# Optimization experiments

Hardware: AMD Instinct MI355X
Metric: run time of the kernel (lower is better)

The kernel has to match this reference:

```python
import jax, jax.numpy as jnp
import numpy as np

B, NQ, NKV = 2, 2048, 2048
DIM, CTX_DIM = 1024, 1024
HEADS, DIM_HEAD = 16, 64
INNER = HEADS * DIM_HEAD  # 1024
SCALE = DIM_HEAD ** -0.5


def setup_inputs() -> dict:
    key = jax.random.key(0)
    ks = jax.random.split(key, 6)
    x = jax.random.normal(ks[0], (B, NQ, DIM), dtype=jnp.float32)
    context = jax.random.normal(ks[1], (B, NKV, CTX_DIM), dtype=jnp.float32)
    # nn.Linear weights stored as [out, in] in torch; we keep [in, out] for x @ W.
    Wq = jax.random.normal(ks[2], (DIM, INNER), dtype=jnp.float32) / np.sqrt(DIM)
    Wkv = jax.random.normal(ks[3], (CTX_DIM, 2 * INNER), dtype=jnp.float32) / np.sqrt(CTX_DIM)
    Wout = jax.random.normal(ks[4], (INNER, DIM), dtype=jnp.float32) / np.sqrt(INNER)
    bout = jax.random.normal(ks[5], (DIM,), dtype=jnp.float32) * 0.01
    return {"x": x, "context": context, "Wq": Wq, "Wkv": Wkv, "Wout": Wout, "bout": bout}


def reference(x, context, Wq, Wkv, Wout, bout):
    q = x @ Wq                      # [B, Nq, inner]
    kv = context @ Wkv              # [B, Nkv, 2*inner]
    k, v = jnp.split(kv, 2, axis=-1)

    def split_heads(t):             # [B, N, inner] -> [B, H, N, dh]
        return t.reshape(t.shape[0], t.shape[1], HEADS, DIM_HEAD).transpose(0, 2, 1, 3)

    q, k, v = split_heads(q), split_heads(k), split_heads(v)
    dots = jnp.einsum('bhqd,bhkd->bhqk', q, k) * SCALE  # [B, H, Nq, Nkv]
    attn = jax.nn.softmax(dots, axis=-1)
    out = jnp.einsum('bhqk,bhkd->bhqd', attn, v)        # [B, H, Nq, dh]
    out = out.transpose(0, 2, 1, 3).reshape(out.shape[0], out.shape[2], INNER)
    return out @ Wout + bout        # [B, Nq, dim]
```

## Files before the change

### kernel.cpp

```cpp
#include <hip/hip_runtime.h>
#include <hip/hip_bf16.h>
#include <stdint.h>

#define NQ 2048
#define NKV 2048
#define DIM 1024
#define INNER 1024
#define HEADS 16
#define DH 64
#define BATCH 2

typedef float f32x4 __attribute__((ext_vector_type(4)));
typedef float f32x16 __attribute__((ext_vector_type(16)));
typedef __bf16 bf16x8 __attribute__((ext_vector_type(8)));
typedef unsigned int u32x4 __attribute__((ext_vector_type(4)));

__device__ inline ushort f2b(float f) {
    uint32_t u = __builtin_bit_cast(uint32_t, f);
    u += 0x7fff + ((u >> 16) & 1);
    return (ushort)(u >> 16);
}

__device__ inline uint pkbf16(float lo, float hi) {
    __hip_bfloat162 h = __float22bfloat162_rn(make_float2(lo, hi));
    uint r;
    __builtin_memcpy(&r, &h, 4);
    return r;
}

__device__ __forceinline__ void gload16(const void* g, void* lds) {
    __builtin_amdgcn_global_load_lds(
        (const __attribute__((address_space(1))) unsigned int*)g,
        (__attribute__((address_space(3))) unsigned int*)lds, 16, 0, 0);
}

__global__ void prep(const float* __restrict__ x, const float* __restrict__ ctx,
                     const float* __restrict__ Wq, const float* __restrict__ Wkv,
                     const float* __restrict__ Wout,
                     ushort* __restrict__ xb, ushort* __restrict__ cb,
                     ushort* __restrict__ Wqt, ushort* __restrict__ Wkvt,
                     ushort* __restrict__ Woutt) {
    int z = blockIdx.z;
    if (z < 4) {
        __shared__ ushort tile[32][33];
        const float* src; ushort* dst; int C;
        if (z == 0)      { src = Wq;          dst = Wqt;                C = 1024; }
        else if (z == 1) { src = Wkv;         dst = Wkvt;               C = 2048; }
        else if (z == 2) { src = Wkv + 1024;  dst = Wkvt + 1024 * 1024; C = 2048; }
        else             { src = Wout;        dst = Woutt;              C = 1024; }
        int c0 = blockIdx.x * 32, r0 = blockIdx.y * 32;
        int tx = threadIdx.x, ty = threadIdx.y;
#pragma unroll
        for (int i = 0; i < 4; i++)
            tile[ty + i * 8][tx] = f2b(src[(size_t)(r0 + ty + i * 8) * C + c0 + tx]);
        __syncthreads();
#pragma unroll
        for (int i = 0; i < 4; i++)
            dst[(size_t)(c0 + ty + i * 8) * 1024 + r0 + tx] = tile[tx][ty + i * 8];
    } else {
        const int n4 = (BATCH * NQ * DIM) / 4;
        int fb = blockIdx.y * 32 + blockIdx.x;
        int t = threadIdx.y * 32 + threadIdx.x;
        for (int i = fb * 256 + t; i < 2 * n4; i += 1024 * 256) {
            float4 v;
            if (i < n4) v = ((const float4*)x)[i];
            else        v = ((const float4*)ctx)[i - n4];
            ushort4 o;
            o.x = f2b(v.x); o.y = f2b(v.y); o.z = f2b(v.z); o.w = f2b(v.w);
            if (i < n4) ((ushort4*)xb)[i] = o;
            else        ((ushort4*)cb)[i - n4] = o;
        }
    }
}

__global__ __launch_bounds__(256) void gemm_qkv(const ushort* __restrict__ xb, const ushort* __restrict__ cb,
                                                const ushort* __restrict__ Wqt, const ushort* __restrict__ Wkvt,
                                                ushort* __restrict__ qb, ushort* __restrict__ kb,
                                                ushort* __restrict__ vtb, float qscale) {
    constexpr int K = 1024, NT = 32;
    __shared__ ushort lds[24576];
    int flat = blockIdx.x;
    int swz = (flat & 7) * 96 + (flat >> 3);
    bool isq = swz < 256;
    const ushort *A, *Bt;
    int m0, n0;
    if (isq) { A = xb; Bt = Wqt;  m0 = (swz >> 3) * 128;  n0 = (swz & 7) * 128; }
    else     { int b2 = swz - 256; A = cb; Bt = Wkvt; m0 = (b2 >> 4) * 128; n0 = (b2 & 15) * 128; }
    int t = threadIdx.x, l = t & 63, w = t >> 6;
    int wr = w >> 1, wc = w & 1;
    int lg = l >> 4, lc = l & 15;
    f32x4 acc[4][4] = {};

    auto stage = [&](int buf, int k0) {
#pragma unroll
        for (int i = 0; i < 2; i++) {
            int s = w + i * 4;
            gload16(A + (size_t)(m0 + (s & 1) * 64 + l) * K + k0 + (s >> 1) * 8, &lds[buf * 8192 + s * 512]);
            gload16(Bt + (size_t)(n0 + (s & 1) * 64 + l) * K + k0 + (s >> 1) * 8, &lds[buf * 8192 + 4096 + s * 512]);
        }
    };

    stage(0, 0);
    stage(1, 32);
    for (int tt = 0; tt < NT; ++tt) {
        int cur = tt % 3;
        if (tt + 2 < NT) {
            stage((tt + 2) % 3, (tt + 2) * 32);
            asm volatile("s_waitcnt vmcnt(8)" ::: "memory");
        } else if (tt + 1 < NT) {
            asm volatile("s_waitcnt vmcnt(4)" ::: "memory");
        } else {
            asm volatile("s_waitcnt vmcnt(0)" ::: "memory");
        }
        __builtin_amdgcn_s_barrier();
        asm volatile("" ::: "memory");
        bf16x8 af[4], bf[4];
#pragma unroll
        for (int mi = 0; mi < 4; mi++)
            af[mi] = *(const bf16x8*)&lds[cur * 8192 + (lg * 128 + wr * 64 + mi * 16 + lc) * 8];
#pragma unroll
        for (int ni = 0; ni < 4; ni++)
            bf[ni] = *(const bf16x8*)&lds[cur * 8192 + 4096 + (lg * 128 + wc * 64 + ni * 16 + lc) * 8];
        __builtin_amdgcn_s_setprio(1);
#pragma unroll
        for (int mi = 0; mi < 4; mi++)
#pragma unroll
            for (int ni = 0; ni < 4; ni++)
                acc[mi][ni] = __builtin_amdgcn_mfma_f32_16x16x32_bf16(af[mi], bf[ni], acc[mi][ni], 0, 0, 0);
        __builtin_amdgcn_s_setprio(0);
        asm volatile("s_waitcnt lgkmcnt(0)" ::: "memory");
        __builtin_amdgcn_s_barrier();
        asm volatile("" ::: "memory");
    }
    if (isq) {
#pragma unroll
        for (int mi = 0; mi < 4; mi++)
#pragma unroll
            for (int ni = 0; ni < 4; ni++)
#pragma unroll
                for (int r = 0; r < 4; r++) {
                    int m = m0 + wr * 64 + mi * 16 + lg * 4 + r;
                    int n = n0 + wc * 64 + ni * 16 + lc;
                    qb[(size_t)m * 1024 + n] = f2b(acc[mi][ni][r] * qscale);
                }
    } else if (n0 < 1024) {
#pragma unroll
        for (int mi = 0; mi < 4; mi++)
#pragma unroll
            for (int ni = 0; ni < 4; ni++)
#pragma unroll
                for (int r = 0; r < 4; r++) {
                    int m = m0 + wr * 64 + mi * 16 + lg * 4 + r;
                    int n = n0 + wc * 64 + ni * 16 + lc;
                    kb[(size_t)m * 1024 + n] = f2b(acc[mi][ni][r]);
                }
    } else {
        int b = m0 >> 11, kv0 = m0 & 2047;
        int h0 = (n0 - 1024) >> 6;
#pragma unroll
        for (int mi = 0; mi < 4; mi++)
#pragma unroll
            for (int ni = 0; ni < 4; ni++)
#pragma unroll
                for (int r = 0; r < 4; r++) {
                    int ml = wr * 64 + mi * 16 + lg * 4 + r;
                    int nl = wc * 64 + ni * 16 + lc;
                    lds[nl * 136 + ml] = f2b(acc[mi][ni][r]);
                }
        __syncthreads();
#pragma unroll
        for (int c = 0; c < 8; c++) {
            int idx = c * 256 + t;
            int rrow = idx >> 4;
            int chunk = idx & 15;
            int h = h0 + (rrow >> 6), d = rrow & 63;
            u32x4 v = *(u32x4*)&lds[rrow * 136 + chunk * 8];
            *(u32x4*)&vtb[(((size_t)b * HEADS + h) * DH + d) * (size_t)NKV + kv0 + chunk * 8] = v;
        }
    }
}

__global__ __launch_bounds__(256) void gemm_out(const ushort* __restrict__ A, const ushort* __restrict__ Bt,
                                                float* __restrict__ C0, const float* __restrict__ bias) {
    constexpr int K = 1024, NT = 32;
    __shared__ ushort lds[24576];
    int flat = blockIdx.x;
    int swz = (flat & 7) * 32 + (flat >> 3);
    int m0 = (swz >> 3) * 128, n0 = (swz & 7) * 128;
    int t = threadIdx.x, l = t & 63, w = t >> 6;
    int wr = w >> 1, wc = w & 1;
    int lg = l >> 4, lc = l & 15;
    f32x4 acc[4][4] = {};

    auto stage = [&](int buf, int k0) {
#pragma unroll
        for (int i = 0; i < 2; i++) {
            int s = w + i * 4;
            gload16(A + (size_t)(m0 + (s & 1) * 64 + l) * K + k0 + (s >> 1) * 8, &lds[buf * 8192 + s * 512]);
            gload16(Bt + (size_t)(n0 + (s & 1) * 64 + l) * K + k0 + (s >> 1) * 8, &lds[buf * 8192 + 4096 + s * 512]);
        }
    };

    stage(0, 0);
    stage(1, 32);
    for (int tt = 0; tt < NT; ++tt) {
        int cur = tt % 3;
        if (tt + 2 < NT) {
            stage((tt + 2) % 3, (tt + 2) * 32);
            asm volatile("s_waitcnt vmcnt(8)" ::: "memory");
        } else if (tt + 1 < NT) {
            asm volatile("s_waitcnt vmcnt(4)" ::: "memory");
        } else {
            asm volatile("s_waitcnt vmcnt(0)" ::: "memory");
        }
        __builtin_amdgcn_s_barrier();
        asm volatile("" ::: "memory");
        bf16x8 af[4], bf[4];
#pragma unroll
        for (int mi = 0; mi < 4; mi++)
            af[mi] = *(const bf16x8*)&lds[cur * 8192 + (lg * 128 + wr * 64 + mi * 16 + lc) * 8];
#pragma unroll
        for (int ni = 0; ni < 4; ni++)
            bf[ni] = *(const bf16x8*)&lds[cur * 8192 + 4096 + (lg * 128 + wc * 64 + ni * 16 + lc) * 8];
        __builtin_amdgcn_s_setprio(1);
#pragma unroll
        for (int mi = 0; mi < 4; mi++)
#pragma unroll
            for (int ni = 0; ni < 4; ni++)
                acc[mi][ni] = __builtin_amdgcn_mfma_f32_16x16x32_bf16(af[mi], bf[ni], acc[mi][ni], 0, 0, 0);
        __builtin_amdgcn_s_setprio(0);
        asm volatile("s_waitcnt lgkmcnt(0)" ::: "memory");
        __builtin_amdgcn_s_barrier();
        asm volatile("" ::: "memory");
    }
#pragma unroll
    for (int mi = 0; mi < 4; mi++)
#pragma unroll
        for (int ni = 0; ni < 4; ni++)
#pragma unroll
            for (int r = 0; r < 4; r++) {
                int m = m0 + wr * 64 + mi * 16 + lg * 4 + r;
                int n = n0 + wc * 64 + ni * 16 + lc;
                C0[(size_t)m * 1024 + n] = acc[mi][ni][r] + bias[n];
            }
}

__global__ __launch_bounds__(256, 2) void attn6(const ushort* __restrict__ qb, const ushort* __restrict__ kb,
                                                const ushort* __restrict__ vtb, ushort* __restrict__ ob) {
    __shared__ ushort Qs[8192];
    __shared__ ushort Ks[3][4096];
    __shared__ ushort Vs[3][4096];
    int flat = blockIdx.x;
    int swz = (flat & 7) * 64 + (flat >> 3);
    int qt = swz & 15, h = (swz >> 4) & 15, b = swz >> 8;
    int t = threadIdx.x, l = t & 63, w = t >> 6;
    int ll = l & 31, hi = l >> 5;
    const ushort* Qg = qb + (size_t)b * NQ * INNER + h * DH;
    const ushort* Kg = kb + (size_t)b * NKV * INNER + h * DH;
    const ushort* Vg = vtb + (((size_t)b * HEADS + h) * DH) * NKV;
    int q0 = qt * 128;

#pragma unroll
    for (int i = 0; i < 4; i++) {
        int s = w * 4 + i;
        gload16(Qg + (size_t)(q0 + (s & 1) * 64 + l) * INNER + (s >> 1) * 8, &Qs[s * 512]);
    }
    auto stageKV = [&](int buf, int kv0) {
#pragma unroll
        for (int i = 0; i < 2; i++) {
            int s = w + i * 4;
            gload16(Kg + (size_t)(kv0 + l) * INNER + s * 8, &Ks[buf][s * 512]);
            gload16(Vg + (size_t)l * NKV + kv0 + s * 8, &Vs[buf][s * 512]);
        }
    };
    stageKV(0, 0);
    stageKV(1, 64);
    asm volatile("s_waitcnt vmcnt(8)" ::: "memory");
    __builtin_amdgcn_s_barrier();
    asm volatile("" ::: "memory");

    bf16x8 qf[4];
#pragma unroll
    for (int dchunk = 0; dchunk < 4; dchunk++) {
        int dc = dchunk * 2 + hi;
        qf[dchunk] = *(const bf16x8*)&Qs[(dc * 128 + w * 32 + ll) * 8];
    }

    f32x16 o0 = {}, o1 = {};
    float m_ = -1e30f, s_ = 0.f;

    constexpr int NT2 = NKV / 64;
    for (int tt = 0; tt < NT2; ++tt) {
        int cur = tt % 3;
        if (tt + 1 < NT2) {
            asm volatile("s_waitcnt vmcnt(4)" ::: "memory");
        } else {
            asm volatile("s_waitcnt vmcnt(0)" ::: "memory");
        }
        __builtin_amdgcn_s_barrier();
        asm volatile("" ::: "memory");
        if (tt + 2 < NT2) stageKV((tt + 2) % 3, (tt + 2) * 64);

        f32x16 st0 = {}, st1 = {};
        __builtin_amdgcn_s_setprio(1);
#pragma unroll
        for (int dchunk = 0; dchunk < 4; dchunk++) {
            int dc = dchunk * 2 + hi;
            bf16x8 kf0 = *(const bf16x8*)&Ks[cur][(dc * 64 + ll) * 8];
            bf16x8 kf1 = *(const bf16x8*)&Ks[cur][(dc * 64 + 32 + ll) * 8];
            st0 = __builtin_amdgcn_mfma_f32_32x32x16_bf16(kf0, qf[dchunk], st0, 0, 0, 0);
            st1 = __builtin_amdgcn_mfma_f32_32x32x16_bf16(kf1, qf[dchunk], st1, 0, 0, 0);
        }
        __builtin_amdgcn_s_setprio(0);

        float mx = st0[0];
#pragma unroll
        for (int r = 1; r < 16; r++) mx = fmaxf(mx, st0[r]);
#pragma unroll
        for (int r = 0; r < 16; r++) mx = fmaxf(mx, st1[r]);
        mx = fmaxf(mx, __shfl_xor(mx, 32));
        if (!__all(mx - m_ <= 8.f)) {
            float mn = fmaxf(m_, mx);
            float fac = __builtin_amdgcn_exp2f(m_ - mn);
            m_ = mn;
            s_ *= fac;
            o0 *= fac;
            o1 *= fac;
        }
        float mn = m_;
        float pp[32];
        float rs = 0.f;
#pragma unroll
        for (int r = 0; r < 16; r++) { pp[r] = __builtin_amdgcn_exp2f(st0[r] - mn); rs += pp[r]; }
#pragma unroll
        for (int r = 0; r < 16; r++) { pp[16 + r] = __builtin_amdgcn_exp2f(st1[r] - mn); rs += pp[16 + r]; }
        rs += __shfl_xor(rs, 32);
        s_ += rs;

        bf16x8 pb[4];
#pragma unroll
        for (int kvb = 0; kvb < 2; kvb++)
#pragma unroll
            for (int c = 0; c < 2; c++) {
                int base = kvb * 16 + c * 8;
                uint a0 = pkbf16(pp[base + 0], pp[base + 1]);
                uint a1 = pkbf16(pp[base + 2], pp[base + 3]);
                uint b0 = pkbf16(pp[base + 4], pp[base + 5]);
                uint b1 = pkbf16(pp[base + 6], pp[base + 7]);
                asm volatile("v_permlane32_swap_b32 %0, %1" : "+v"(a0), "+v"(b0));
                asm volatile("v_permlane32_swap_b32 %0, %1" : "+v"(a1), "+v"(b1));
                u32x4 wrd = {a0, a1, b0, b1};
                pb[kvb * 2 + c] = __builtin_bit_cast(bf16x8, wrd);
            }

        __builtin_amdgcn_s_setprio(1);
#pragma unroll
        for (int kvchunk = 0; kvchunk < 4; kvchunk++) {
            int kvc = kvchunk * 2 + hi;
            bf16x8 vf0 = *(const bf16x8*)&Vs[cur][(kvc * 64 + ll) * 8];
            bf16x8 vf1 = *(const bf16x8*)&Vs[cur][(kvc * 64 + 32 + ll) * 8];
            o0 = __builtin_amdgcn_mfma_f32_32x32x16_bf16(vf0, pb[kvchunk], o0, 0, 0, 0);
            o1 = __builtin_amdgcn_mfma_f32_32x32x16_bf16(vf1, pb[kvchunk], o1, 0, 0, 0);
        }
        __builtin_amdgcn_s_setprio(0);
    }

    ushort* Og = ob + (size_t)b * NQ * INNER + h * DH;
    float inv = 1.f / s_;
    int q = q0 + w * 32 + ll;
#pragma unroll
    for (int rq = 0; rq < 4; rq++) {
        int d0 = 8 * rq + 4 * hi;
        uint2 pw;
        pw.x = pkbf16(o0[4 * rq + 0] * inv, o0[4 * rq + 1] * inv);
        pw.y = pkbf16(o0[4 * rq + 2] * inv, o0[4 * rq + 3] * inv);
        *(uint2*)&Og[(size_t)q * INNER + d0] = pw;
        uint2 pw1;
        pw1.x = pkbf16(o1[4 * rq + 0] * inv, o1[4 * rq + 1] * inv);
        pw1.y = pkbf16(o1[4 * rq + 2] * inv, o1[4 * rq + 3] * inv);
        *(uint2*)&Og[(size_t)q * INNER + 32 + d0] = pw1;
    }
}

extern "C" void kernel_launch(void* const* d_in, const int* in_sizes, int n_in,
                              void* d_out, int out_size, void* d_ws, size_t ws_size,
                              hipStream_t stream) {
    const float* x    = (const float*)d_in[0];
    const float* ctx  = (const float*)d_in[1];
    const float* Wq   = (const float*)d_in[2];
    const float* Wkv  = (const float*)d_in[3];
    const float* Wout = (const float*)d_in[4];
    const float* bout = (const float*)d_in[5];
    float* out = (float*)d_out;

    if (ws_size < (size_t)(56u << 20)) return;
    char* ws = (char*)d_ws;
    ushort* xb    = (ushort*)(ws);
    ushort* cb    = (ushort*)(ws + (8u << 20));
    ushort* ob    = (ushort*)(ws + (8u << 20));
    ushort* qb    = (ushort*)(ws + (16u << 20));
    ushort* kb    = (ushort*)(ws + (24u << 20));
    ushort* vtb   = (ushort*)(ws + (32u << 20));
    ushort* Wqt   = (ushort*)(ws + (48u << 20));
    ushort* Wkvt  = (ushort*)(ws + (50u << 20));
    ushort* Woutt = (ushort*)(ws + (54u << 20));

    prep<<<dim3(32, 32, 5), dim3(32, 8), 0, stream>>>(x, ctx, Wq, Wkv, Wout, xb, cb, Wqt, Wkvt, Woutt);
    gemm_qkv<<<768, 256, 0, stream>>>(xb, cb, Wqt, Wkvt, qb, kb, vtb, 0.125f * 1.44269504f);
    attn6<<<512, 256, 0, stream>>>(qb, kb, vtb, ob);
    gemm_out<<<256, 256, 0, stream>>>(ob, Woutt, out, bout);
}
```

Baseline: 160.9 us.

## Software-pipeline QK^T with softmax in attention, deepen KV buffering, halve out-GEMM tile

The attention kernel now computes the next tile's QK^T scores before running softmax and PV on the current tile, alternating two score register sets so matrix-core work overlaps the exp and reduction math. KV staging goes from three to four LDS buffers with a prefetch distance of three, and Q is loaded straight from global memory into registers, dropping its LDS buffer. The max and sum reductions become balanced trees. The output GEMM uses 64x128 tiles with 512 blocks for better CU fill, at the cost of more register pressure in attention and less B reuse in the GEMM.

Result: slower. 168.0 us (+4.4%).

```diff
diff --git a/kernel.cpp b/kernel.cpp
--- a/kernel.cpp
+++ b/kernel.cpp
@@ -183,21 +183,21 @@
 __global__ __launch_bounds__(256) void gemm_out(const ushort* __restrict__ A, const ushort* __restrict__ Bt,
                                                 float* __restrict__ C0, const float* __restrict__ bias) {
     constexpr int K = 1024, NT = 32;
-    __shared__ ushort lds[24576];
+    __shared__ ushort lds[3][6144];
     int flat = blockIdx.x;
-    int swz = (flat & 7) * 32 + (flat >> 3);
-    int m0 = (swz >> 3) * 128, n0 = (swz & 7) * 128;
+    int swz = (flat & 7) * 64 + (flat >> 3);
+    int m0 = (swz >> 3) * 64, n0 = (swz & 7) * 128;
     int t = threadIdx.x, l = t & 63, w = t >> 6;
     int wr = w >> 1, wc = w & 1;
     int lg = l >> 4, lc = l & 15;
-    f32x4 acc[4][4] = {};
+    f32x4 acc[2][4] = {};
 
     auto stage = [&](int buf, int k0) {
+        gload16(A + (size_t)(m0 + l) * K + k0 + w * 8, &lds[buf][w * 512 + l * 8]);
 #pragma unroll
         for (int i = 0; i < 2; i++) {
             int s = w + i * 4;
-            gload16(A + (size_t)(m0 + (s & 1) * 64 + l) * K + k0 + (s >> 1) * 8, &lds[buf * 8192 + s * 512]);
-            gload16(Bt + (size_t)(n0 + (s & 1) * 64 + l) * K + k0 + (s >> 1) * 8, &lds[buf * 8192 + 4096 + s * 512]);
+            gload16(Bt + (size_t)(n0 + (s & 1) * 64 + l) * K + k0 + (s >> 1) * 8, &lds[buf][2048 + s * 512]);
         }
     };
 
@@ -207,24 +207,24 @@
         int cur = tt % 3;
         if (tt + 2 < NT) {
             stage((tt + 2) % 3, (tt + 2) * 32);
-            asm volatile("s_waitcnt vmcnt(8)" ::: "memory");
+            asm volatile("s_waitcnt vmcnt(6)" ::: "memory");
         } else if (tt + 1 < NT) {
-            asm volatile("s_waitcnt vmcnt(4)" ::: "memory");
+            asm volatile("s_waitcnt vmcnt(3)" ::: "memory");
         } else {
             asm volatile("s_waitcnt vmcnt(0)" ::: "memory");
         }
         __builtin_amdgcn_s_barrier();
         asm volatile("" ::: "memory");
-        bf16x8 af[4], bf[4];
-#pragma unroll
-        for (int mi = 0; mi < 4; mi++)
-            af[mi] = *(const bf16x8*)&lds[cur * 8192 + (lg * 128 + wr * 64 + mi * 16 + lc) * 8];
+        bf16x8 af[2], bf[4];
+#pragma unroll
+        for (int mi = 0; mi < 2; mi++)
+            af[mi] = *(const bf16x8*)&lds[cur][(lg * 64 + wr * 32 + mi * 16 + lc) * 8];
 #pragma unroll
         for (int ni = 0; ni < 4; ni++)
-            bf[ni] = *(const bf16x8*)&lds[cur * 8192 + 4096 + (lg * 128 + wc * 64 + ni * 16 + lc) * 8];
+            bf[ni] = *(const bf16x8*)&lds[cur][2048 + (lg * 128 + wc * 64 + ni * 16 + lc) * 8];
         __builtin_amdgcn_s_setprio(1);
 #pragma unroll
-        for (int mi = 0; mi < 4; mi++)
+        for (int mi = 0; mi < 2; mi++)
 #pragma unroll
             for (int ni = 0; ni < 4; ni++)
                 acc[mi][ni] = __builtin_amdgcn_mfma_f32_16x16x32_bf16(af[mi], bf[ni], acc[mi][ni], 0, 0, 0);
@@ -234,22 +234,21 @@
         asm volatile("" ::: "memory");
     }
 #pragma unroll
-    for (int mi = 0; mi < 4; mi++)
+    for (int mi = 0; mi < 2; mi++)
 #pragma unroll
         for (int ni = 0; ni < 4; ni++)
 #pragma unroll
             for (int r = 0; r < 4; r++) {
-                int m = m0 + wr * 64 + mi * 16 + lg * 4 + r;
+                int m = m0 + wr * 32 + mi * 16 + lg * 4 + r;
                 int n = n0 + wc * 64 + ni * 16 + lc;
                 C0[(size_t)m * 1024 + n] = acc[mi][ni][r] + bias[n];
             }
 }
 
-__global__ __launch_bounds__(256, 2) void attn6(const ushort* __restrict__ qb, const ushort* __restrict__ kb,
+__global__ __launch_bounds__(256, 2) void attn7(const ushort* __restrict__ qb, const ushort* __restrict__ kb,
                                                 const ushort* __restrict__ vtb, ushort* __restrict__ ob) {
-    __shared__ ushort Qs[8192];
-    __shared__ ushort Ks[3][4096];
-    __shared__ ushort Vs[3][4096];
+    __shared__ ushort Ks[4][4096];
+    __shared__ ushort Vs[4][4096];
     int flat = blockIdx.x;
     int swz = (flat & 7) * 64 + (flat >> 3);
     int qt = swz & 15, h = (swz >> 4) & 15, b = swz >> 8;
@@ -259,11 +258,13 @@
     const ushort* Kg = kb + (size_t)b * NKV * INNER + h * DH;
     const ushort* Vg = vtb + (((size_t)b * HEADS + h) * DH) * NKV;
     int q0 = qt * 128;
-
-#pragma unroll
-    for (int i = 0; i < 4; i++) {
-        int s = w * 4 + i;
-        gload16(Qg + (size_t)(q0 + (s & 1) * 64 + l) * INNER + (s >> 1) * 8, &Qs[s * 512]);
+    constexpr int NT2 = NKV / 64;
+
+    bf16x8 qf[4];
+#pragma unroll
+    for (int dchunk = 0; dchunk < 4; dchunk++) {
+        int dc = dchunk * 2 + hi;
+        qf[dchunk] = *(const bf16x8*)&Qg[(size_t)(q0 + w * 32 + ll) * INNER + dc * 8];
     }
     auto stageKV = [&](int buf, int kv0) {
 #pragma unroll
@@ -273,67 +274,75 @@
             gload16(Vg + (size_t)l * NKV + kv0 + s * 8, &Vs[buf][s * 512]);
         }
     };
-    stageKV(0, 0);
-    stageKV(1, 64);
+    stageKV(0, 0); stageKV(1, 64); stageKV(2, 128);
     asm volatile("s_waitcnt vmcnt(8)" ::: "memory");
     __builtin_amdgcn_s_barrier();
     asm volatile("" ::: "memory");
 
-    bf16x8 qf[4];
-#pragma unroll
-    for (int dchunk = 0; dchunk < 4; dchunk++) {
-        int dc = dchunk * 2 + hi;
-        qf[dchunk] = *(const bf16x8*)&Qs[(dc * 128 + w * 32 + ll) * 8];
-    }
+    f32x16 zf = {};
+    auto qk = [&](f32x16& d0, f32x16& d1, int bufi) {
+        d0 = zf; d1 = zf;
+        __builtin_amdgcn_s_setprio(1);
+#pragma unroll
+        for (int dchunk = 0; dchunk < 4; dchunk++) {
+            int dc = dchunk * 2 + hi;
+            bf16x8 kf0 = *(const bf16x8*)&Ks[bufi][(dc * 64 + ll) * 8];
+            bf16x8 kf1 = *(const bf16x8*)&Ks[bufi][(dc * 64 + 32 + ll) * 8];
+            d0 = __builtin_amdgcn_mfma_f32_32x32x16_bf16(kf0, qf[dchunk], d0, 0, 0, 0);
+            d1 = __builtin_amdgcn_mfma_f32_32x32x16_bf16(kf1, qf[dchunk], d1, 0, 0, 0);
+        }
+        __builtin_amdgcn_s_setprio(0);
+    };
+
+    f32x16 stA0, stA1, stB0, stB1;
+    qk(stA0, stA1, 0);
 
     f32x16 o0 = {}, o1 = {};
     float m_ = -1e30f, s_ = 0.f;
 
-    constexpr int NT2 = NKV / 64;
-    for (int tt = 0; tt < NT2; ++tt) {
-        int cur = tt % 3;
-        if (tt + 1 < NT2) {
-            asm volatile("s_waitcnt vmcnt(4)" ::: "memory");
-        } else {
-            asm volatile("s_waitcnt vmcnt(0)" ::: "memory");
-        }
+    auto body = [&](f32x16& c0, f32x16& c1, f32x16& n0v, f32x16& n1v, int tt) {
+        if (tt + 2 < NT2) { asm volatile("s_waitcnt vmcnt(4)" ::: "memory"); }
+        else              { asm volatile("s_waitcnt vmcnt(0)" ::: "memory"); }
         __builtin_amdgcn_s_barrier();
         asm volatile("" ::: "memory");
-        if (tt + 2 < NT2) stageKV((tt + 2) % 3, (tt + 2) * 64);
-
-        f32x16 st0 = {}, st1 = {};
-        __builtin_amdgcn_s_setprio(1);
-#pragma unroll
-        for (int dchunk = 0; dchunk < 4; dchunk++) {
-            int dc = dchunk * 2 + hi;
-            bf16x8 kf0 = *(const bf16x8*)&Ks[cur][(dc * 64 + ll) * 8];
-            bf16x8 kf1 = *(const bf16x8*)&Ks[cur][(dc * 64 + 32 + ll) * 8];
-            st0 = __builtin_amdgcn_mfma_f32_32x32x16_bf16(kf0, qf[dchunk], st0, 0, 0, 0);
-            st1 = __builtin_amdgcn_mfma_f32_32x32x16_bf16(kf1, qf[dchunk], st1, 0, 0, 0);
-        }
-        __builtin_amdgcn_s_setprio(0);
-
-        float mx = st0[0];
-#pragma unroll
-        for (int r = 1; r < 16; r++) mx = fmaxf(mx, st0[r]);
-#pragma unroll
-        for (int r = 0; r < 16; r++) mx = fmaxf(mx, st1[r]);
+        if (tt + 3 < NT2) stageKV((tt + 3) & 3, (tt + 3) * 64);
+        if (tt + 1 < NT2) qk(n0v, n1v, (tt + 1) & 3);
+
+        float mx;
+        {
+            float a = fmaxf(fmaxf(c0[0], c0[1]), fmaxf(c0[2], c0[3]));
+            float b2 = fmaxf(fmaxf(c0[4], c0[5]), fmaxf(c0[6], c0[7]));
+            float c = fmaxf(fmaxf(c0[8], c0[9]), fmaxf(c0[10], c0[11]));
+            float d = fmaxf(fmaxf(c0[12], c0[13]), fmaxf(c0[14], c0[15]));
+            float e = fmaxf(fmaxf(c1[0], c1[1]), fmaxf(c1[2], c1[3]));
+            float f = fmaxf(fmaxf(c1[4], c1[5]), fmaxf(c1[6], c1[7]));
+            float g = fmaxf(fmaxf(c1[8], c1[9]), fmaxf(c1[10], c1[11]));
+            float h2 = fmaxf(fmaxf(c1[12], c1[13]), fmaxf(c1[14], c1[15]));
+            mx = fmaxf(fmaxf(fmaxf(a, b2), fmaxf(c, d)), fmaxf(fmaxf(e, f), fmaxf(g, h2)));
+        }
         mx = fmaxf(mx, __shfl_xor(mx, 32));
         if (!__all(mx - m_ <= 8.f)) {
-            float mn = fmaxf(m_, mx);
-            float fac = __builtin_amdgcn_exp2f(m_ - mn);
-            m_ = mn;
-            s_ *= fac;
-            o0 *= fac;
-            o1 *= fac;
+            float mn2 = fmaxf(m_, mx);
+            float fac = __builtin_amdgcn_exp2f(m_ - mn2);
+            m_ = mn2; s_ *= fac; o0 *= fac; o1 *= fac;
         }
         float mn = m_;
-        float pp[32];
-        float rs = 0.f;
-#pragma unroll
-        for (int r = 0; r < 16; r++) { pp[r] = __builtin_amdgcn_exp2f(st0[r] - mn); rs += pp[r]; }
-#pragma unroll
-        for (int r = 0; r < 16; r++) { pp[16 + r] = __builtin_amdgcn_exp2f(st1[r] - mn); rs += pp[16 + r]; }
+#pragma unroll
+        for (int r = 0; r < 16; r++) c0[r] = __builtin_amdgcn_exp2f(c0[r] - mn);
+#pragma unroll
+        for (int r = 0; r < 16; r++) c1[r] = __builtin_amdgcn_exp2f(c1[r] - mn);
+        float rs;
+        {
+            float a = (c0[0] + c0[1]) + (c0[2] + c0[3]);
+            float b2 = (c0[4] + c0[5]) + (c0[6] + c0[7]);
+            float c = (c0[8] + c0[9]) + (c0[10] + c0[11]);
+            float d = (c0[12] + c0[13]) + (c0[14] + c0[15]);
+            float e = (c1[0] + c1[1]) + (c1[2] + c1[3]);
+            float f = (c1[4] + c1[5]) + (c1[6] + c1[7]);
+            float g = (c1[8] + c1[9]) + (c1[10] + c1[11]);
+            float h2 = (c1[12] + c1[13]) + (c1[14] + c1[15]);
+            rs = ((a + b2) + (c + d)) + ((e + f) + (g + h2));
+        }
         rs += __shfl_xor(rs, 32);
         s_ += rs;
 
@@ -342,11 +351,15 @@
         for (int kvb = 0; kvb < 2; kvb++)
 #pragma unroll
             for (int c = 0; c < 2; c++) {
-                int base = kvb * 16 + c * 8;
-                uint a0 = pkbf16(pp[base + 0], pp[base + 1]);
-                uint a1 = pkbf16(pp[base + 2], pp[base + 3]);
-                uint b0 = pkbf16(pp[base + 4], pp[base + 5]);
-                uint b1 = pkbf16(pp[base + 6], pp[base + 7]);
+                int base = c * 8;
+                uint a0, a1, b0, b1;
+                if (kvb == 0) {
+                    a0 = pkbf16(c0[base + 0], c0[base + 1]); a1 = pkbf16(c0[base + 2], c0[base + 3]);
+                    b0 = pkbf16(c0[base + 4], c0[base + 5]); b1 = pkbf16(c0[base + 6], c0[base + 7]);
+                } else {
+                    a0 = pkbf16(c1[base + 0], c1[base + 1]); a1 = pkbf16(c1[base + 2], c1[base + 3]);
+                    b0 = pkbf16(c1[base + 4], c1[base + 5]); b1 = pkbf16(c1[base + 6], c1[base + 7]);
+                }
                 asm volatile("v_permlane32_swap_b32 %0, %1" : "+v"(a0), "+v"(b0));
                 asm volatile("v_permlane32_swap_b32 %0, %1" : "+v"(a1), "+v"(b1));
                 u32x4 wrd = {a0, a1, b0, b1};
@@ -357,12 +370,17 @@
 #pragma unroll
         for (int kvchunk = 0; kvchunk < 4; kvchunk++) {
             int kvc = kvchunk * 2 + hi;
-            bf16x8 vf0 = *(const bf16x8*)&Vs[cur][(kvc * 64 + ll) * 8];
-            bf16x8 vf1 = *(const bf16x8*)&Vs[cur][(kvc * 64 + 32 + ll) * 8];
+            bf16x8 vf0 = *(const bf16x8*)&Vs[tt & 3][(kvc * 64 + ll) * 8];
+            bf16x8 vf1 = *(const bf16x8*)&Vs[tt & 3][(kvc * 64 + 32 + ll) * 8];
             o0 = __builtin_amdgcn_mfma_f32_32x32x16_bf16(vf0, pb[kvchunk], o0, 0, 0, 0);
             o1 = __builtin_amdgcn_mfma_f32_32x32x16_bf16(vf1, pb[kvchunk], o1, 0, 0, 0);
         }
         __builtin_amdgcn_s_setprio(0);
+    };
+
+    for (int tt = 0; tt < NT2; tt += 2) {
+        body(stA0, stA1, stB0, stB1, tt);
+        body(stB0, stB1, stA0, stA1, tt + 1);
     }
 
     ushort* Og = ob + (size_t)b * NQ * INNER + h * DH;
@@ -407,6 +425,6 @@
 
     prep<<<dim3(32, 32, 5), dim3(32, 8), 0, stream>>>(x, ctx, Wq, Wkv, Wout, xb, cb, Wqt, Wkvt, Woutt);
     gemm_qkv<<<768, 256, 0, stream>>>(xb, cb, Wqt, Wkvt, qb, kb, vtb, 0.125f * 1.44269504f);
-    attn6<<<512, 256, 0, stream>>>(qb, kb, vtb, ob);
-    gemm_out<<<256, 256, 0, stream>>>(ob, Woutt, out, bout);
-}
+    attn7<<<512, 256, 0, stream>>>(qb, kb, vtb, ob);
+    gemm_out<<<512, 256, 0, stream>>>(ob, Woutt, out, bout);
+}
```

## Process 128-wide KV tiles per iteration with double-buffered pairs and direct Q loads

Applied to the files above, without the earlier changes.

The attention kernel now handles two 64-row KV tiles per loop iteration, using a 4-slot LDS ring organised as two ping-pong pairs. This halves the number of barriers and softmax max/rescale checks per KV element. Q fragments are read straight from global memory into registers instead of being staged through LDS, and the max and sum reductions use tree-shaped vector ops. In exchange the kernel holds more live registers for four score tiles, and with only one pair in flight ahead it waits on vmcnt(0) every iteration, which may expose global-load latency.

Measured after the change: 163.8 us. Within noise of the previous version (+1.8%).

```diff
diff --git a/kernel.cpp b/kernel.cpp
--- a/kernel.cpp
+++ b/kernel.cpp
@@ -245,11 +245,10 @@
             }
 }
 
-__global__ __launch_bounds__(256, 2) void attn6(const ushort* __restrict__ qb, const ushort* __restrict__ kb,
+__global__ __launch_bounds__(256, 2) void attn8(const ushort* __restrict__ qb, const ushort* __restrict__ kb,
                                                 const ushort* __restrict__ vtb, ushort* __restrict__ ob) {
-    __shared__ ushort Qs[8192];
-    __shared__ ushort Ks[3][4096];
-    __shared__ ushort Vs[3][4096];
+    __shared__ ushort Ks[4][4096];
+    __shared__ ushort Vs[4][4096];
     int flat = blockIdx.x;
     int swz = (flat & 7) * 64 + (flat >> 3);
     int qt = swz & 15, h = (swz >> 4) & 15, b = swz >> 8;
@@ -259,11 +258,13 @@
     const ushort* Kg = kb + (size_t)b * NKV * INNER + h * DH;
     const ushort* Vg = vtb + (((size_t)b * HEADS + h) * DH) * NKV;
     int q0 = qt * 128;
-
-#pragma unroll
-    for (int i = 0; i < 4; i++) {
-        int s = w * 4 + i;
-        gload16(Qg + (size_t)(q0 + (s & 1) * 64 + l) * INNER + (s >> 1) * 8, &Qs[s * 512]);
+    constexpr int NP = NKV / 128;
+
+    bf16x8 qf[4];
+#pragma unroll
+    for (int dchunk = 0; dchunk < 4; dchunk++) {
+        int dc = dchunk * 2 + hi;
+        qf[dchunk] = *(const bf16x8*)&Qg[(size_t)(q0 + w * 32 + ll) * INNER + dc * 8];
     }
     auto stageKV = [&](int buf, int kv0) {
 #pragma unroll
@@ -273,94 +274,127 @@
             gload16(Vg + (size_t)l * NKV + kv0 + s * 8, &Vs[buf][s * 512]);
         }
     };
-    stageKV(0, 0);
-    stageKV(1, 64);
-    asm volatile("s_waitcnt vmcnt(8)" ::: "memory");
-    __builtin_amdgcn_s_barrier();
-    asm volatile("" ::: "memory");
-
-    bf16x8 qf[4];
-#pragma unroll
-    for (int dchunk = 0; dchunk < 4; dchunk++) {
-        int dc = dchunk * 2 + hi;
-        qf[dchunk] = *(const bf16x8*)&Qs[(dc * 128 + w * 32 + ll) * 8];
-    }
+    stageKV(0, 0); stageKV(1, 64);
+    stageKV(2, 128); stageKV(3, 192);
 
     f32x16 o0 = {}, o1 = {};
     float m_ = -1e30f, s_ = 0.f;
-
-    constexpr int NT2 = NKV / 64;
-    for (int tt = 0; tt < NT2; ++tt) {
-        int cur = tt % 3;
-        if (tt + 1 < NT2) {
-            asm volatile("s_waitcnt vmcnt(4)" ::: "memory");
-        } else {
-            asm volatile("s_waitcnt vmcnt(0)" ::: "memory");
-        }
+    f32x16 zf = {};
+
+    for (int tt = 0; tt < NP; ++tt) {
+        int cur0 = (tt & 1) << 1;
+        int cur1 = cur0 + 1;
+        if (tt == 0) { asm volatile("s_waitcnt vmcnt(8)" ::: "memory"); }
+        else         { asm volatile("s_waitcnt vmcnt(0)" ::: "memory"); }
         __builtin_amdgcn_s_barrier();
         asm volatile("" ::: "memory");
-        if (tt + 2 < NT2) stageKV((tt + 2) % 3, (tt + 2) * 64);
-
-        f32x16 st0 = {}, st1 = {};
+        if (tt + 1 < NP) {
+            int nb0 = (cur0 ^ 2);
+            stageKV(nb0, (tt + 1) * 128);
+            stageKV(nb0 + 1, (tt + 1) * 128 + 64);
+        }
+
+        f32x16 sA0 = zf, sA1 = zf, sB0 = zf, sB1 = zf;
         __builtin_amdgcn_s_setprio(1);
 #pragma unroll
         for (int dchunk = 0; dchunk < 4; dchunk++) {
             int dc = dchunk * 2 + hi;
-            bf16x8 kf0 = *(const bf16x8*)&Ks[cur][(dc * 64 + ll) * 8];
-            bf16x8 kf1 = *(const bf16x8*)&Ks[cur][(dc * 64 + 32 + ll) * 8];
-            st0 = __builtin_amdgcn_mfma_f32_32x32x16_bf16(kf0, qf[dchunk], st0, 0, 0, 0);
-            st1 = __builtin_amdgcn_mfma_f32_32x32x16_bf16(kf1, qf[dchunk], st1, 0, 0, 0);
+            bf16x8 ka0 = *(const bf16x8*)&Ks[cur0][(dc * 64 + ll) * 8];
+            bf16x8 ka1 = *(const bf16x8*)&Ks[cur0][(dc * 64 + 32 + ll) * 8];
+            bf16x8 kb0 = *(const bf16x8*)&Ks[cur1][(dc * 64 + ll) * 8];
+            bf16x8 kb1 = *(const bf16x8*)&Ks[cur1][(dc * 64 + 32 + ll) * 8];
+            sA0 = __builtin_amdgcn_mfma_f32_32x32x16_bf16(ka0, qf[dchunk], sA0, 0, 0, 0);
+            sA1 = __builtin_amdgcn_mfma_f32_32x32x16_bf16(ka1, qf[dchunk], sA1, 0, 0, 0);
+            sB0 = __builtin_amdgcn_mfma_f32_32x32x16_bf16(kb0, qf[dchunk], sB0, 0, 0, 0);
+            sB1 = __builtin_amdgcn_mfma_f32_32x32x16_bf16(kb1, qf[dchunk], sB1, 0, 0, 0);
         }
         __builtin_amdgcn_s_setprio(0);
 
-        float mx = st0[0];
-#pragma unroll
-        for (int r = 1; r < 16; r++) mx = fmaxf(mx, st0[r]);
-#pragma unroll
-        for (int r = 0; r < 16; r++) mx = fmaxf(mx, st1[r]);
+        float mx;
+        {
+            f32x16 m01 = __builtin_elementwise_max(__builtin_elementwise_max(sA0, sA1),
+                                                   __builtin_elementwise_max(sB0, sB1));
+            float a = fmaxf(fmaxf(m01[0], m01[1]), fmaxf(m01[2], m01[3]));
+            float b2 = fmaxf(fmaxf(m01[4], m01[5]), fmaxf(m01[6], m01[7]));
+            float c = fmaxf(fmaxf(m01[8], m01[9]), fmaxf(m01[10], m01[11]));
+            float d = fmaxf(fmaxf(m01[12], m01[13]), fmaxf(m01[14], m01[15]));
+            mx = fmaxf(fmaxf(a, b2), fmaxf(c, d));
+        }
         mx = fmaxf(mx, __shfl_xor(mx, 32));
         if (!__all(mx - m_ <= 8.f)) {
-            float mn = fmaxf(m_, mx);
-            float fac = __builtin_amdgcn_exp2f(m_ - mn);
-            m_ = mn;
-            s_ *= fac;
-            o0 *= fac;
-            o1 *= fac;
+            float mn2 = fmaxf(m_, mx);
+            float fac = __builtin_amdgcn_exp2f(m_ - mn2);
+            m_ = mn2; s_ *= fac; o0 *= fac; o1 *= fac;
         }
         float mn = m_;
-        float pp[32];
-        float rs = 0.f;
-#pragma unroll
-        for (int r = 0; r < 16; r++) { pp[r] = __builtin_amdgcn_exp2f(st0[r] - mn); rs += pp[r]; }
-#pragma unroll
-        for (int r = 0; r < 16; r++) { pp[16 + r] = __builtin_amdgcn_exp2f(st1[r] - mn); rs += pp[16 + r]; }
+#pragma unroll
+        for (int r = 0; r < 16; r++) sA0[r] = __builtin_amdgcn_exp2f(sA0[r] - mn);
+#pragma unroll
+        for (int r = 0; r < 16; r++) sA1[r] = __builtin_amdgcn_exp2f(sA1[r] - mn);
+#pragma unroll
+        for (int r = 0; r < 16; r++) sB0[r] = __builtin_amdgcn_exp2f(sB0[r] - mn);
+#pragma unroll
+        for (int r = 0; r < 16; r++) sB1[r] = __builtin_amdgcn_exp2f(sB1[r] - mn);
+        float rs;
+        {
+            f32x16 sm = (sA0 + sA1) + (sB0 + sB1);
+            float a = (sm[0] + sm[1]) + (sm[2] + sm[3]);
+            float b2 = (sm[4] + sm[5]) + (sm[6] + sm[7]);
+            float c = (sm[8] + sm[9]) + (sm[10] + sm[11]);
+            float d = (sm[12] + sm[13]) + (sm[14] + sm[15]);
+            rs = (a + b2) + (c + d);
+        }
         rs += __shfl_xor(rs, 32);
         s_ += rs;
 
-        bf16x8 pb[4];
+        bf16x8 pbA[4], pbB[4];
 #pragma unroll
         for (int kvb = 0; kvb < 2; kvb++)
 #pragma unroll
             for (int c = 0; c < 2; c++) {
-                int base = kvb * 16 + c * 8;
-                uint a0 = pkbf16(pp[base + 0], pp[base + 1]);
-                uint a1 = pkbf16(pp[base + 2], pp[base + 3]);
-                uint b0 = pkbf16(pp[base + 4], pp[base + 5]);
-                uint b1 = pkbf16(pp[base + 6], pp[base + 7]);
+                int base = c * 8;
+                const f32x16& s0 = (kvb == 0) ? sA0 : sA1;
+                uint a0 = pkbf16(s0[base + 0], s0[base + 1]);
+                uint a1 = pkbf16(s0[base + 2], s0[base + 3]);
+                uint b0 = pkbf16(s0[base + 4], s0[base + 5]);
+                uint b1 = pkbf16(s0[base + 6], s0[base + 7]);
                 asm volatile("v_permlane32_swap_b32 %0, %1" : "+v"(a0), "+v"(b0));
                 asm volatile("v_permlane32_swap_b32 %0, %1" : "+v"(a1), "+v"(b1));
                 u32x4 wrd = {a0, a1, b0, b1};
-                pb[kvb * 2 + c] = __builtin_bit_cast(bf16x8, wrd);
+                pbA[kvb * 2 + c] = __builtin_bit_cast(bf16x8, wrd);
+            }
+#pragma unroll
+        for (int kvb = 0; kvb < 2; kvb++)
+#pragma unroll
+            for (int c = 0; c < 2; c++) {
+                int base = c * 8;
+                const f32x16& s0 = (kvb == 0) ? sB0 : sB1;
+                uint a0 = pkbf16(s0[base + 0], s0[base + 1]);
+                uint a1 = pkbf16(s0[base + 2], s0[base + 3]);
+                uint b0 = pkbf16(s0[base + 4], s0[base + 5]);
+                uint b1 = pkbf16(s0[base + 6], s0[base + 7]);
+                asm volatile("v_permlane32_swap_b32 %0, %1" : "+v"(a0), "+v"(b0));
+                asm volatile("v_permlane32_swap_b32 %0, %1" : "+v"(a1), "+v"(b1));
+                u32x4 wrd = {a0, a1, b0, b1};
+                pbB[kvb * 2 + c] = __builtin_bit_cast(bf16x8, wrd);
             }
 
         __builtin_amdgcn_s_setprio(1);
 #pragma unroll
         for (int kvchunk = 0; kvchunk < 4; kvchunk++) {
             int kvc = kvchunk * 2 + hi;
-            bf16x8 vf0 = *(const bf16x8*)&Vs[cur][(kvc * 64 + ll) * 8];
-            bf16x8 vf1 = *(const bf16x8*)&Vs[cur][(kvc * 64 + 32 + ll) * 8];
-            o0 = __builtin_amdgcn_mfma_f32_32x32x16_bf16(vf0, pb[kvchunk], o0, 0, 0, 0);
-            o1 = __builtin_amdgcn_mfma_f32_32x32x16_bf16(vf1, pb[kvchunk], o1, 0, 0, 0);
+            bf16x8 va0 = *(const bf16x8*)&Vs[cur0][(kvc * 64 + ll) * 8];
+            bf16x8 va1 = *(const bf16x8*)&Vs[cur0][(kvc * 64 + 32 + ll) * 8];
+            o0 = __builtin_amdgcn_mfma_f32_32x32x16_bf16(va0, pbA[kvchunk], o0, 0, 0, 0);
+            o1 = __builtin_amdgcn_mfma_f32_32x32x16_bf16(va1, pbA[kvchunk], o1, 0, 0, 0);
+        }
+#pragma unroll
+        for (int kvchunk = 0; kvchunk < 4; kvchunk++) {
+            int kvc = kvchunk * 2 + hi;
+            bf16x8 vb0 = *(const bf16x8*)&Vs[cur1][(kvc * 64 + ll) * 8];
+            bf16x8 vb1 = *(const bf16x8*)&Vs[cur1][(kvc * 64 + 32 + ll) * 8];
+            o0 = __builtin_amdgcn_mfma_f32_32x32x16_bf16(vb0, pbB[kvchunk], o0, 0, 0, 0);
+            o1 = __builtin_amdgcn_mfma_f32_32x32x16_bf16(vb1, pbB[kvchunk], o1, 0, 0, 0);
         }
         __builtin_amdgcn_s_setprio(0);
     }
@@ -407,6 +441,6 @@
 
     prep<<<dim3(32, 32, 5), dim3(32, 8), 0, stream>>>(x, ctx, Wq, Wkv, Wout, xb, cb, Wqt, Wkvt, Woutt);
     gemm_qkv<<<768, 256, 0, stream>>>(xb, cb, Wqt, Wkvt, qb, kb, vtb, 0.125f * 1.44269504f);
-    attn6<<<512, 256, 0, stream>>>(qb, kb, vtb, ob);
+    attn8<<<512, 256, 0, stream>>>(qb, kb, vtb, ob);
     gemm_out<<<256, 256, 0, stream>>>(ob, Woutt, out, bout);
 }
```
